# Performance work log

Measured on AMD Instinct MI355X. Metric: run time of the kernel, lower is better.

The kernel has to match this reference:

```python
import jax, jax.numpy as jnp
import numpy as np
from jax import lax

DIM = 128
HEADS = 8
HEAD_DIM = DIM // HEADS
SR = 2
B, H, W = 2, 80, 80
SCALE = HEAD_DIM ** (-0.5)
BN_EPS = 1e-5


def _conv1x1(x, w, b):
    # x: (B,C,H,W), w: (O,C), b: (O,)
    return jnp.einsum('bchw,oc->bohw', x, w) + b[None, :, None, None]


def setup_inputs() -> dict:
    key = jax.random.key(0)
    ks = jax.random.split(key, 12)
    s = DIM ** -0.5
    x = jax.random.normal(ks[0], (B, DIM, H, W), dtype=jnp.float32)
    q_w = jax.random.normal(ks[1], (DIM, DIM), dtype=jnp.float32) * s
    q_b = jnp.zeros((DIM,), jnp.float32)
    k_w = jax.random.normal(ks[2], (DIM, DIM), dtype=jnp.float32) * s
    k_b = jnp.zeros((DIM,), jnp.float32)
    v_w = jax.random.normal(ks[3], (DIM, DIM), dtype=jnp.float32) * s
    v_b = jnp.zeros((DIM,), jnp.float32)
    sr_w = jax.random.normal(ks[4], (DIM, DIM, SR, SR), dtype=jnp.float32) * (s / SR)
    sr_b = jnp.zeros((DIM,), jnp.float32)
    bn_gamma = jnp.ones((DIM,), jnp.float32)
    bn_beta = jnp.zeros((DIM,), jnp.float32)
    bn_mean = jnp.zeros((DIM,), jnp.float32)
    bn_var = jnp.ones((DIM,), jnp.float32)
    proj_w = jax.random.normal(ks[5], (DIM, DIM), dtype=jnp.float32) * s
    proj_b = jnp.zeros((DIM,), jnp.float32)
    return dict(x=x, q_w=q_w, q_b=q_b, k_w=k_w, k_b=k_b, v_w=v_w, v_b=v_b,
                sr_w=sr_w, sr_b=sr_b, bn_gamma=bn_gamma, bn_beta=bn_beta,
                bn_mean=bn_mean, bn_var=bn_var, proj_w=proj_w, proj_b=proj_b)


def reference(x, q_w, q_b, k_w, k_b, v_w, v_b, sr_w, sr_b,
              bn_gamma, bn_beta, bn_mean, bn_var, proj_w, proj_b):
    b, c, h, w = x.shape
    n = h * w
    # q: (B,h,N,d)
    q = _conv1x1(x, q_w, q_b).reshape(b, HEADS, HEAD_DIM, n).transpose(0, 1, 3, 2)
    # spatial reduction: Conv2d(k=SR, s=SR) + BN(eval) + ReLU
    x_kv = lax.conv_general_dilated(x, sr_w, window_strides=(SR, SR),
                                    padding='VALID',
                                    dimension_numbers=('NCHW', 'OIHW', 'NCHW'))
    x_kv = x_kv + sr_b[None, :, None, None]
    inv = bn_gamma / jnp.sqrt(bn_var + BN_EPS)
    x_kv = x_kv * inv[None, :, None, None] + (bn_beta - bn_mean * inv)[None, :, None, None]
    x_kv = jax.nn.relu(x_kv)
    n_kv = x_kv.shape[2] * x_kv.shape[3]
    k = _conv1x1(x_kv, k_w, k_b).reshape(b, HEADS, HEAD_DIM, n_kv).transpose(0, 1, 3, 2)
    v = _conv1x1(x_kv, v_w, v_b).reshape(b, HEADS, HEAD_DIM, n_kv).transpose(0, 1, 3, 2)
    # explicit attention: (B,h,N,N_kv)
    attn = jnp.einsum('bhnd,bhmd->bhnm', q, k) * SCALE
    attn = jax.nn.softmax(attn, axis=-1)
    out = jnp.einsum('bhnm,bhmd->bhnd', attn, v)  # (B,h,N,d)
    # faithful to source layout: transpose(1,2) then reshape to (B,C,H,W)
    out = out.transpose(0, 2, 1, 3).reshape(b, c, h, w)
    out = _conv1x1(out, proj_w, proj_b)
    return out
```

## Files before the change

### kernel.cpp

```cpp
#include <hip/hip_runtime.h>
#include <hip/hip_bf16.h>
#include <cmath>

#define DIM 128
#define HEADS 8
#define HEAD_DIM 16
#define NBATCH 2
#define HH 80
#define WW 80
#define NQ 6400
#define NKV 1600
#define NC 50
#define BN_EPS 1e-5f
#define LOG2E 1.4426950408889634f

typedef __bf16 bf16_t;
typedef __attribute__((ext_vector_type(8))) __bf16 bf16x8;
typedef __attribute__((ext_vector_type(16))) float f32x16;

union BF8U { bf16x8 v; unsigned u[4]; };

__device__ inline unsigned packbf2(float a, float b) {
  union { __hip_bfloat162 v; unsigned u; } r;
  r.v = __float22bfloat162_rn(make_float2(a, b));
  return r.u;
}

__device__ inline unsigned short f2bf(float v) {
  unsigned u = __float_as_uint(v);
  return (unsigned short)((u + 0x7FFFu + ((u >> 16) & 1u)) >> 16);
}

__global__ void xpose_x(const float* __restrict__ x, unsigned short* __restrict__ Xb)
{
  int s0 = blockIdx.x * 32, c0 = blockIdx.y * 32, b = blockIdx.z;
  __shared__ float tile[32][33];
#pragma unroll
  for (int r = 0; r < 32; r += 8)
    tile[threadIdx.y + r][threadIdx.x] =
        x[((size_t)b * DIM + c0 + threadIdx.y + r) * NQ + s0 + threadIdx.x];
  __syncthreads();
#pragma unroll
  for (int r = 0; r < 32; r += 8)
    Xb[((size_t)b * NQ + s0 + threadIdx.y + r) * DIM + c0 + threadIdx.x] =
        f2bf(tile[threadIdx.x][threadIdx.y + r]);
}

__global__ void prep(const float* __restrict__ x,
                     const float* __restrict__ qw, const float* __restrict__ kw,
                     const float* __restrict__ vw, const float* __restrict__ pw,
                     const float* __restrict__ srw,
                     unsigned short* __restrict__ Wb,
                     unsigned short* __restrict__ X4b,
                     unsigned short* __restrict__ Vp)
{
  int e = blockIdx.x * 256 + threadIdx.x;
  if (e < 131072) {
    const float* src; int idx;
    if (e < 16384)      { src = qw;  idx = e; }
    else if (e < 32768) { src = kw;  idx = e - 16384; }
    else if (e < 49152) { src = vw;  idx = e - 32768; }
    else if (e < 65536) { src = pw;  idx = e - 49152; }
    else                { src = srw; idx = e - 65536; }
    Wb[e] = f2bf(src[idx]);
  }
  if (e < NBATCH * HEADS * NC * 32) {
    int cid = e >> 5;
    int pos = e & 31;
    size_t addr = (size_t)cid * 1024 + 256 + ((pos & 16) ? 512 : 0) + (pos & 15);
    Vp[addr] = 0x3F80;
  }
  int c4 = e & 511;
  int r = e >> 9;
  int b = r / 1600, m = r % 1600;
  int c = c4 >> 2, ky = (c4 >> 1) & 1, kx = c4 & 1;
  int i = m / 40, j = m % 40;
  X4b[e] = f2bf(x[((size_t)b * DIM + c) * NQ + (2 * i + ky) * WW + 2 * j + kx]);
}

__global__ __launch_bounds__(256) void mgemm_qsr(
    const bf16_t* __restrict__ Xb, const bf16_t* __restrict__ X4b,
    const bf16_t* __restrict__ Wb,
    const float* __restrict__ q_b, const float* __restrict__ sr_b,
    unsigned short* __restrict__ Qb, unsigned short* __restrict__ xkvb,
    float sl,
    const float* __restrict__ bng, const float* __restrict__ bnb,
    const float* __restrict__ bnm, const float* __restrict__ bnv)
{
  int t = threadIdx.x;
  int ln = t & 31, hf = (t >> 5) & 1, wid = t >> 6;
  int b = blockIdx.y;
  bool isq = blockIdx.x < 200;
  int s0 = isq ? blockIdx.x * 32 : (blockIdx.x - 200) * 32;
  int S  = isq ? NQ : NKV;
  int C  = isq ? 128 : 512;
  const bf16_t* X = isq ? Xb : X4b;
  const bf16_t* W = isq ? Wb : (Wb + 65536);
  int o = wid * 32 + ln;

  const bf16_t* arow = &X[((size_t)b * S + s0 + ln) * C + hf * 8];
  const bf16_t* brow = &W[(size_t)o * C + hf * 8];
  f32x16 acc = {};
#pragma unroll 8
  for (int c0 = 0; c0 < C; c0 += 16) {
    bf16x8 af = *(const bf16x8*)&arow[c0];
    bf16x8 bf = *(const bf16x8*)&brow[c0];
    acc = __builtin_amdgcn_mfma_f32_32x32x16_bf16(af, bf, acc, 0, 0, 0);
  }

  float bv, a1, b2;
  bool relu;
  if (isq) { bv = q_b[o]; a1 = sl; b2 = 0.f; relu = false; }
  else {
    bv = sr_b[o];
    float inv = bng[o] / sqrtf(bnv[o] + BN_EPS);
    a1 = inv; b2 = bnb[o] - bnm[o] * inv; relu = true;
  }
  unsigned short* ob = isq ? Qb : xkvb;
#pragma unroll
  for (int g = 0; g < 4; ++g)
#pragma unroll
    for (int j = 0; j < 4; ++j) {
      float v = (acc[4 * g + j] + bv) * a1 + b2;
      if (relu) v = fmaxf(v, 0.f);
      int s = s0 + 8 * g + 4 * hf + j;
      ob[((size_t)b * S + s) * DIM + o] = f2bf(v);
    }
}

__global__ __launch_bounds__(256) void mgemm_kv(
    const bf16_t* __restrict__ xkvb, const bf16_t* __restrict__ Wb,
    const float* __restrict__ k_b, const float* __restrict__ v_b,
    unsigned short* __restrict__ Kp, unsigned short* __restrict__ Vp)
{
  int t = threadIdx.x;
  int ln = t & 31, hf = (t >> 5) & 1, wid = t >> 6;
  int b = blockIdx.y;
  int isv = blockIdx.z;
  int s0 = blockIdx.x * 32;
  const bf16_t* W = Wb + (isv ? 32768 : 16384);
  int o = wid * 32 + ln;

  const bf16_t* arow = &xkvb[((size_t)b * NKV + s0 + ln) * DIM + hf * 8];
  const bf16_t* brow = &W[(size_t)o * DIM + hf * 8];
  f32x16 acc = {};
#pragma unroll
  for (int c0 = 0; c0 < 128; c0 += 16) {
    bf16x8 af = *(const bf16x8*)&arow[c0];
    bf16x8 bf = *(const bf16x8*)&brow[c0];
    acc = __builtin_amdgcn_mfma_f32_32x32x16_bf16(af, bf, acc, 0, 0, 0);
  }

  int hloc = o >> 4, d = o & 15;
  if (isv) {
    float bv = v_b[o];
    size_t CB = (((size_t)b * HEADS + hloc) * NC + (s0 >> 5)) * 1024;
    uint4 w0, w1;
    w0.x = packbf2(acc[0] + bv, acc[1] + bv);
    w0.y = packbf2(acc[2] + bv, acc[3] + bv);
    w0.z = packbf2(acc[4] + bv, acc[5] + bv);
    w0.w = packbf2(acc[6] + bv, acc[7] + bv);
    w1.x = packbf2(acc[8] + bv, acc[9] + bv);
    w1.y = packbf2(acc[10] + bv, acc[11] + bv);
    w1.z = packbf2(acc[12] + bv, acc[13] + bv);
    w1.w = packbf2(acc[14] + bv, acc[15] + bv);
    *(uint4*)&Vp[CB + d * 16 + hf * 8] = w0;
    *(uint4*)&Vp[CB + 512 + d * 16 + hf * 8] = w1;
  } else {
    float bv = k_b[o];
    size_t CB = (((size_t)b * HEADS + hloc) * NC + (s0 >> 5)) * 512;
#pragma unroll
    for (int g = 0; g < 4; ++g)
#pragma unroll
      for (int j = 0; j < 4; ++j) {
        int sl2 = 8 * g + 4 * hf + j;
        Kp[CB + sl2 * 16 + d] = f2bf(acc[4 * g + j] + bv);
      }
  }
}

__global__ __launch_bounds__(64) void attn_split(const bf16_t* __restrict__ Qb,
                                                 const bf16_t* __restrict__ Kp,
                                                 const bf16_t* __restrict__ Vp,
                                                 unsigned short* __restrict__ Pb,
                                                 float* __restrict__ Lsum)
{
  const int t = threadIdx.x;
  const int ln = t & 31, hf = t >> 5;
  const int h = blockIdx.y;
  const int b = blockIdx.z & 1, half = blockIdx.z >> 1;
  const int q0 = blockIdx.x * 32;

  bf16x8 qf = *(const bf16x8*)&Qb[((size_t)b * NQ + q0 + ln) * 128 + h * 16 + hf * 8];
  const int bh = b * HEADS + h;
  const bf16_t* kc = &Kp[((size_t)bh * NC + half * 25) * 512 + ln * 16 + hf * 8];
  const bf16_t* vc = &Vp[((size_t)bh * NC + half * 25) * 1024 + ln * 16 + hf * 8];

  f32x16 acc = {};
  const f32x16 zero = {};

  bf16x8 kf = *(const bf16x8*)kc;
  bf16x8 va = *(const bf16x8*)vc;
  bf16x8 vb = *(const bf16x8*)(vc + 512);

  for (int c = 0; c < 25; ++c) {
    int cn = (c < 24) ? c + 1 : c;
    bf16x8 kf2 = *(const bf16x8*)(kc + cn * 512);
    bf16x8 va2 = *(const bf16x8*)(vc + cn * 1024);
    bf16x8 vb2 = *(const bf16x8*)(vc + cn * 1024 + 512);

    f32x16 S = __builtin_amdgcn_mfma_f32_32x32x16_bf16(kf, qf, zero, 0, 0, 0);

    BF8U f0, f1;
#pragma unroll
    for (int i = 0; i < 4; ++i) {
      f0.u[i] = packbf2(__builtin_amdgcn_exp2f(S[2 * i]),
                        __builtin_amdgcn_exp2f(S[2 * i + 1]));
      f1.u[i] = packbf2(__builtin_amdgcn_exp2f(S[8 + 2 * i]),
                        __builtin_amdgcn_exp2f(S[9 + 2 * i]));
    }

    acc = __builtin_amdgcn_mfma_f32_32x32x16_bf16(va, f0.v, acc, 0, 0, 0);
    acc = __builtin_amdgcn_mfma_f32_32x32x16_bf16(vb, f1.v, acc, 0, 0, 0);
    kf = kf2; va = va2; vb = vb2;
  }

  unsigned short* prow =
      &Pb[(((size_t)(half * 2 + b)) * NQ + q0 + ln) * 128 + h * 16 + 4 * hf];
  uint2 w0, w1;
  w0.x = packbf2(acc[0], acc[1]); w0.y = packbf2(acc[2], acc[3]);
  w1.x = packbf2(acc[4], acc[5]); w1.y = packbf2(acc[6], acc[7]);
  *(uint2*)&prow[0] = w0;
  *(uint2*)&prow[8] = w1;
  if (!hf)
    Lsum[(((size_t)(half * 2 + b)) * HEADS + h) * NQ + q0 + ln] = acc[8];
}

__global__ void combine_s(const unsigned short* __restrict__ Pb,
                          const float* __restrict__ Lsum,
                          unsigned short* __restrict__ P2)
{
  int s0 = blockIdx.x * 32, c0 = blockIdx.y * 32, b = blockIdx.z;
  int tx = threadIdx.x, ty = threadIdx.y;
  __shared__ float tile[32][33];
#pragma unroll
  for (int r = 0; r < 32; r += 8) {
    int c = c0 + ty + r;
    int f = c * NQ + s0 + tx;
    int n = f >> 7, hh = (f >> 4) & 7;
    float p0 = __uint_as_float((unsigned)Pb[(size_t)b * 819200 + f] << 16);
    float p1 = __uint_as_float((unsigned)Pb[(size_t)(2 + b) * 819200 + f] << 16);
    float L = Lsum[((size_t)b * HEADS + hh) * NQ + n] +
              Lsum[((size_t)(2 + b) * HEADS + hh) * NQ + n];
    tile[ty + r][tx] = (p0 + p1) / L;
  }
  __syncthreads();
#pragma unroll
  for (int r = 0; r < 32; r += 8)
    P2[(size_t)b * 819200 + (size_t)(s0 + ty + r) * 128 + c0 + tx] =
        f2bf(tile[tx][ty + r]);
}

__global__ __launch_bounds__(256) void proj_gemm(const bf16_t* __restrict__ P2,
                                                 const bf16_t* __restrict__ Wb,
                                                 const float* __restrict__ bias,
                                                 float* __restrict__ Out)
{
  int t = threadIdx.x;
  int ln = t & 31, hf = (t >> 5) & 1, wid = t >> 6;
  int b = blockIdx.y;
  int s0 = blockIdx.x * 32;
  int o = wid * 32 + ln;
  const bf16_t* arow = &P2[((size_t)b * NQ + s0 + ln) * DIM + hf * 8];
  const bf16_t* brow = &Wb[49152 + (size_t)o * DIM + hf * 8];
  f32x16 acc = {};
#pragma unroll
  for (int c0 = 0; c0 < 128; c0 += 16) {
    bf16x8 af = *(const bf16x8*)&arow[c0];
    bf16x8 bf = *(const bf16x8*)&brow[c0];
    acc = __builtin_amdgcn_mfma_f32_32x32x16_bf16(af, bf, acc, 0, 0, 0);
  }
  float bv = bias[o];
  float* obase = &Out[((size_t)b * DIM + o) * NQ + s0 + 4 * hf];
#pragma unroll
  for (int g = 0; g < 4; ++g) {
    float4 r;
    r.x = acc[4 * g + 0] + bv; r.y = acc[4 * g + 1] + bv;
    r.z = acc[4 * g + 2] + bv; r.w = acc[4 * g + 3] + bv;
    *(float4*)&obase[8 * g] = r;
  }
}

extern "C" void kernel_launch(void* const* d_in, const int* in_sizes, int n_in,
                              void* d_out, int out_size, void* d_ws, size_t ws_size,
                              hipStream_t stream)
{
  const float* x    = (const float*)d_in[0];
  const float* q_w  = (const float*)d_in[1];
  const float* q_b  = (const float*)d_in[2];
  const float* k_w  = (const float*)d_in[3];
  const float* k_b  = (const float*)d_in[4];
  const float* v_w  = (const float*)d_in[5];
  const float* v_b  = (const float*)d_in[6];
  const float* sr_w = (const float*)d_in[7];
  const float* sr_b = (const float*)d_in[8];
  const float* bng  = (const float*)d_in[9];
  const float* bnb  = (const float*)d_in[10];
  const float* bnm  = (const float*)d_in[11];
  const float* bnv  = (const float*)d_in[12];
  const float* p_w  = (const float*)d_in[13];
  const float* p_b  = (const float*)d_in[14];
  float* out = (float*)d_out;

  float* ws = (float*)d_ws;
  bf16_t* Xb   = (bf16_t*)(ws);
  bf16_t* X4b  = (bf16_t*)(ws + 819200);
  bf16_t* xkvb = (bf16_t*)(ws + 1638400);
  bf16_t* Pb   = (bf16_t*)(ws);
  bf16_t* Qb   = (bf16_t*)(ws + 1843200);
  bf16_t* P2   = (bf16_t*)(ws + 1843200);
  bf16_t* Kp   = (bf16_t*)(ws + 2662400);
  bf16_t* Vp   = (bf16_t*)(ws + 2867200);
  float*  Lsum = ws + 3276800;
  bf16_t* Wb   = (bf16_t*)(ws + 3481600);

  const float sl = 0.25f * LOG2E;

  xpose_x<<<dim3(200, 4, 2), dim3(32, 8), 0, stream>>>(x, (unsigned short*)Xb);

  prep<<<dim3(6400), dim3(256), 0, stream>>>(
      x, q_w, k_w, v_w, p_w, sr_w,
      (unsigned short*)Wb, (unsigned short*)X4b, (unsigned short*)Vp);

  mgemm_qsr<<<dim3(250, NBATCH), dim3(256), 0, stream>>>(
      Xb, X4b, Wb, q_b, sr_b, (unsigned short*)Qb, (unsigned short*)xkvb,
      sl, bng, bnb, bnm, bnv);

  mgemm_kv<<<dim3(NKV / 32, NBATCH, 2), dim3(256), 0, stream>>>(
      xkvb, Wb, k_b, v_b, (unsigned short*)Kp, (unsigned short*)Vp);

  attn_split<<<dim3(NQ / 32, HEADS, 4), dim3(64), 0, stream>>>(
      Qb, Kp, Vp, (unsigned short*)Pb, Lsum);

  combine_s<<<dim3(200, 4, 2), dim3(32, 8), 0, stream>>>(
      (const unsigned short*)Pb, Lsum, (unsigned short*)P2);

  proj_gemm<<<dim3(NQ / 32, NBATCH), dim3(256), 0, stream>>>(
      P2, Wb, p_b, out);
}
```

Measured before the change: 165.3 us.

## Fuse transpose into prep, merge combine into projection, widen attention blocks

Merges the x transpose kernel into the prep kernel through block-index dispatch. It also folds the split-softmax combine step into the projection GEMM, staging normalized bf16 activations in shared memory, which removes the P2 intermediate and one global round trip. The attention kernel now runs four waves per block covering 128 queries instead of one wave per block. Together these cut two kernel launches and some global traffic. The cost is that the combine now does strided gathers inside the projection block, and there are fewer, larger attention blocks.

```diff
diff --git a/kernel.cpp b/kernel.cpp
--- a/kernel.cpp
+++ b/kernel.cpp
@@ -31,30 +31,34 @@
   return (unsigned short)((u + 0x7FFFu + ((u >> 16) & 1u)) >> 16);
 }
 
-__global__ void xpose_x(const float* __restrict__ x, unsigned short* __restrict__ Xb)
-{
-  int s0 = blockIdx.x * 32, c0 = blockIdx.y * 32, b = blockIdx.z;
+__global__ __launch_bounds__(256) void prep_all(
+    const float* __restrict__ x,
+    const float* __restrict__ qw, const float* __restrict__ kw,
+    const float* __restrict__ vw, const float* __restrict__ pw,
+    const float* __restrict__ srw,
+    unsigned short* __restrict__ Xb,
+    unsigned short* __restrict__ Wb,
+    unsigned short* __restrict__ X4b,
+    unsigned short* __restrict__ Vp)
+{
   __shared__ float tile[32][33];
-#pragma unroll
-  for (int r = 0; r < 32; r += 8)
-    tile[threadIdx.y + r][threadIdx.x] =
-        x[((size_t)b * DIM + c0 + threadIdx.y + r) * NQ + s0 + threadIdx.x];
-  __syncthreads();
-#pragma unroll
-  for (int r = 0; r < 32; r += 8)
-    Xb[((size_t)b * NQ + s0 + threadIdx.y + r) * DIM + c0 + threadIdx.x] =
-        f2bf(tile[threadIdx.x][threadIdx.y + r]);
-}
-
-__global__ void prep(const float* __restrict__ x,
-                     const float* __restrict__ qw, const float* __restrict__ kw,
-                     const float* __restrict__ vw, const float* __restrict__ pw,
-                     const float* __restrict__ srw,
-                     unsigned short* __restrict__ Wb,
-                     unsigned short* __restrict__ X4b,
-                     unsigned short* __restrict__ Vp)
-{
-  int e = blockIdx.x * 256 + threadIdx.x;
+  int t = threadIdx.x;
+  int bx = blockIdx.x;
+  if (bx < 1600) {
+    int tx = t & 31, ty = t >> 5;
+    int b = bx / 800;
+    int rem = bx % 800;
+    int c0 = (rem / 200) * 32, s0 = (rem % 200) * 32;
+#pragma unroll
+    for (int r = 0; r < 32; r += 8)
+      tile[ty + r][tx] = x[((size_t)b * DIM + c0 + ty + r) * NQ + s0 + tx];
+    __syncthreads();
+#pragma unroll
+    for (int r = 0; r < 32; r += 8)
+      Xb[((size_t)b * NQ + s0 + ty + r) * DIM + c0 + tx] = f2bf(tile[tx][ty + r]);
+    return;
+  }
+  int e = (bx - 1600) * 256 + t;
   if (e < 131072) {
     const float* src; int idx;
     if (e < 16384)      { src = qw;  idx = e; }
@@ -179,17 +183,17 @@
   }
 }
 
-__global__ __launch_bounds__(64) void attn_split(const bf16_t* __restrict__ Qb,
-                                                 const bf16_t* __restrict__ Kp,
-                                                 const bf16_t* __restrict__ Vp,
-                                                 unsigned short* __restrict__ Pb,
-                                                 float* __restrict__ Lsum)
+__global__ __launch_bounds__(256) void attn_split(const bf16_t* __restrict__ Qb,
+                                                  const bf16_t* __restrict__ Kp,
+                                                  const bf16_t* __restrict__ Vp,
+                                                  unsigned short* __restrict__ Pb,
+                                                  float* __restrict__ Lsum)
 {
   const int t = threadIdx.x;
-  const int ln = t & 31, hf = t >> 5;
+  const int ln = t & 31, hf = (t >> 5) & 1, wid = t >> 6;
   const int h = blockIdx.y;
   const int b = blockIdx.z & 1, half = blockIdx.z >> 1;
-  const int q0 = blockIdx.x * 32;
+  const int q0 = blockIdx.x * 128 + wid * 32;
 
   bf16x8 qf = *(const bf16x8*)&Qb[((size_t)b * NQ + q0 + ln) * 128 + h * 16 + hf * 8];
   const int bh = b * HEADS + h;
@@ -236,43 +240,37 @@
     Lsum[(((size_t)(half * 2 + b)) * HEADS + h) * NQ + q0 + ln] = acc[8];
 }
 
-__global__ void combine_s(const unsigned short* __restrict__ Pb,
-                          const float* __restrict__ Lsum,
-                          unsigned short* __restrict__ P2)
-{
-  int s0 = blockIdx.x * 32, c0 = blockIdx.y * 32, b = blockIdx.z;
-  int tx = threadIdx.x, ty = threadIdx.y;
-  __shared__ float tile[32][33];
-#pragma unroll
-  for (int r = 0; r < 32; r += 8) {
-    int c = c0 + ty + r;
-    int f = c * NQ + s0 + tx;
-    int n = f >> 7, hh = (f >> 4) & 7;
-    float p0 = __uint_as_float((unsigned)Pb[(size_t)b * 819200 + f] << 16);
-    float p1 = __uint_as_float((unsigned)Pb[(size_t)(2 + b) * 819200 + f] << 16);
-    float L = Lsum[((size_t)b * HEADS + hh) * NQ + n] +
-              Lsum[((size_t)(2 + b) * HEADS + hh) * NQ + n];
-    tile[ty + r][tx] = (p0 + p1) / L;
-  }
-  __syncthreads();
-#pragma unroll
-  for (int r = 0; r < 32; r += 8)
-    P2[(size_t)b * 819200 + (size_t)(s0 + ty + r) * 128 + c0 + tx] =
-        f2bf(tile[tx][ty + r]);
-}
-
-__global__ __launch_bounds__(256) void proj_gemm(const bf16_t* __restrict__ P2,
+__global__ __launch_bounds__(256) void proj_comb(const unsigned short* __restrict__ Pb,
+                                                 const float* __restrict__ Lsum,
                                                  const bf16_t* __restrict__ Wb,
                                                  const float* __restrict__ bias,
                                                  float* __restrict__ Out)
 {
+  __shared__ unsigned short As[32][136];
   int t = threadIdx.x;
-  int ln = t & 31, hf = (t >> 5) & 1, wid = t >> 6;
   int b = blockIdx.y;
   int s0 = blockIdx.x * 32;
+
+  {
+    int tx = t & 31, cg = t >> 5;
+#pragma unroll
+    for (int it = 0; it < 16; ++it) {
+      int c = cg * 16 + it;
+      int f = c * NQ + s0 + tx;
+      int n = f >> 7, hh = (f >> 4) & 7;
+      float p0 = __uint_as_float((unsigned)Pb[(size_t)b * 819200 + f] << 16);
+      float p1 = __uint_as_float((unsigned)Pb[(size_t)(2 + b) * 819200 + f] << 16);
+      float L = Lsum[((size_t)b * HEADS + hh) * NQ + n] +
+                Lsum[((size_t)(2 + b) * HEADS + hh) * NQ + n];
+      As[tx][c] = f2bf((p0 + p1) / L);
+    }
+  }
+  __syncthreads();
+
+  int ln = t & 31, hf = (t >> 5) & 1, wid = t >> 6;
   int o = wid * 32 + ln;
-  const bf16_t* arow = &P2[((size_t)b * NQ + s0 + ln) * DIM + hf * 8];
   const bf16_t* brow = &Wb[49152 + (size_t)o * DIM + hf * 8];
+  const unsigned short* arow = &As[ln][hf * 8];
   f32x16 acc = {};
 #pragma unroll
   for (int c0 = 0; c0 < 128; c0 += 16) {
@@ -318,7 +316,6 @@
   bf16_t* xkvb = (bf16_t*)(ws + 1638400);
   bf16_t* Pb   = (bf16_t*)(ws);
   bf16_t* Qb   = (bf16_t*)(ws + 1843200);
-  bf16_t* P2   = (bf16_t*)(ws + 1843200);
   bf16_t* Kp   = (bf16_t*)(ws + 2662400);
   bf16_t* Vp   = (bf16_t*)(ws + 2867200);
   float*  Lsum = ws + 3276800;
@@ -326,11 +323,10 @@
 
   const float sl = 0.25f * LOG2E;
 
-  xpose_x<<<dim3(200, 4, 2), dim3(32, 8), 0, stream>>>(x, (unsigned short*)Xb);
-
-  prep<<<dim3(6400), dim3(256), 0, stream>>>(
+  prep_all<<<dim3(8000), dim3(256), 0, stream>>>(
       x, q_w, k_w, v_w, p_w, sr_w,
-      (unsigned short*)Wb, (unsigned short*)X4b, (unsigned short*)Vp);
+      (unsigned short*)Xb, (unsigned short*)Wb,
+      (unsigned short*)X4b, (unsigned short*)Vp);
 
   mgemm_qsr<<<dim3(250, NBATCH), dim3(256), 0, stream>>>(
       Xb, X4b, Wb, q_b, sr_b, (unsigned short*)Qb, (unsigned short*)xkvb,
@@ -339,12 +335,9 @@
   mgemm_kv<<<dim3(NKV / 32, NBATCH, 2), dim3(256), 0, stream>>>(
       xkvb, Wb, k_b, v_b, (unsigned short*)Kp, (unsigned short*)Vp);
 
-  attn_split<<<dim3(NQ / 32, HEADS, 4), dim3(64), 0, stream>>>(
+  attn_split<<<dim3(NQ / 128, HEADS, 4), dim3(256), 0, stream>>>(
       Qb, Kp, Vp, (unsigned short*)Pb, Lsum);
 
-  combine_s<<<dim3(200, 4, 2), dim3(32, 8), 0, stream>>>(
-      (const unsigned short*)Pb, Lsum, (unsigned short*)P2);
-
-  proj_gemm<<<dim3(NQ / 32, NBATCH), dim3(256), 0, stream>>>(
-      P2, Wb, p_b, out);
-}
+  proj_comb<<<dim3(200, NBATCH), dim3(256), 0, stream>>>(
+      (const unsigned short*)Pb, Lsum, Wb, p_b, out);
+}
```

Result: faster. 161.5 us (-2.3%).
